# Performance work log

Measured on AMD Instinct MI355X. Metric: run time of the kernel, lower is better.

The kernel has to match this reference:

```python
import jax, jax.numpy as jnp
import numpy as np

ALPHA = 0.2  # leaky relu slope
NEG = -9e15

N, NFEAT, NHID, NHEADS = 4096, 1024, 64, 8
EMB = NHID * NHEADS  # 512


def setup_inputs() -> dict:
    key = jax.random.key(0)
    ks = jax.random.split(key, 16)
    x = jax.random.normal(ks[0], (N, NFEAT), dtype=jnp.float32)
    adj = (jax.random.uniform(ks[1], (N, N)) < 0.01).astype(jnp.float32)
    adj = jnp.maximum(adj, jnp.eye(N, dtype=jnp.float32))
    s = 0.05
    W = jax.random.normal(ks[2], (NHEADS, NFEAT, NHID), dtype=jnp.float32) * s
    a1 = jax.random.normal(ks[3], (NHEADS, NHID), dtype=jnp.float32) * s
    a2 = jax.random.normal(ks[4], (NHEADS, NHID), dtype=jnp.float32) * s
    # decoder: 512 -> 256 -> 256 -> 512 -> 1024 (PyTorch Linear convention: y = x @ W.T + b)
    W1 = jax.random.normal(ks[5], (EMB // 2, EMB), dtype=jnp.float32) * s
    b1 = jnp.zeros((EMB // 2,), dtype=jnp.float32)
    W2 = jax.random.normal(ks[6], (NFEAT // 4, EMB // 2), dtype=jnp.float32) * s
    b2 = jnp.zeros((NFEAT // 4,), dtype=jnp.float32)
    W3 = jax.random.normal(ks[7], (NFEAT // 2, NFEAT // 4), dtype=jnp.float32) * s
    b3 = jnp.zeros((NFEAT // 2,), dtype=jnp.float32)
    W4 = jax.random.normal(ks[8], (NFEAT, NFEAT // 2), dtype=jnp.float32) * s
    b4 = jnp.zeros((NFEAT,), dtype=jnp.float32)
    return {"x": x, "adj": adj, "W": W, "a1": a1, "a2": a2,
            "W1": W1, "b1": b1, "W2": W2, "b2": b2,
            "W3": W3, "b3": b3, "W4": W4, "b4": b4}


def reference(x, adj, W, a1, a2, W1, b1, W2, b2, W3, b3, W4, b4):
    # --- encoder: multi-head GAT (dropout=0) ---
    Wh = jnp.einsum('nf,hfd->hnd', x, W)              # [H, N, nhid]
    e_src = jnp.einsum('hnd,hd->hn', Wh, a1)          # [H, N]
    e_dst = jnp.einsum('hnd,hd->hn', Wh, a2)          # [H, N]
    e = jax.nn.leaky_relu(e_src[:, :, None] + e_dst[:, None, :], ALPHA)  # [H, N, N]
    e = jnp.where(adj[None] > 0, e, NEG)
    att = jax.nn.softmax(e, axis=-1)
    h = jnp.einsum('hnm,hmd->hnd', att, Wh)           # [H, N, nhid]
    h = jax.nn.elu(h)                                 # concat=True -> elu per layer
    enc = jnp.transpose(h, (1, 0, 2)).reshape(x.shape[0], -1)  # [N, H*nhid]
    # --- decoder: 4-layer MLP ---
    out = jax.nn.relu(enc @ W1.T + b1)
    out = jax.nn.relu(out @ W2.T + b2)
    out = jax.nn.relu(out @ W3.T + b3)
    out = out @ W4.T + b4
    return out
```

## Files before the change

### kernel.cpp

```cpp
#include <hip/hip_runtime.h>
#include <hip/hip_bf16.h>
#include <math.h>

#define NNODES 4096
#define NFEAT_ 1024
#define NHID_  64
#define NHEADS_ 8
#define EMB_   512
#define MAXD   256
constexpr float ALPHA_ = 0.2f;

typedef __attribute__((ext_vector_type(8))) short bf16x8;
typedef __attribute__((ext_vector_type(4))) float f32x4;
typedef unsigned int u32;
typedef unsigned short u16;

__device__ inline u16 f2b(float f) {
    __hip_bfloat16 b = __float2bfloat16(f);
    return *(u16*)&b;
}
__device__ inline float b2f(u16 u) {
    return __uint_as_float(((u32)u) << 16);
}

__device__ inline void cp16(const void* g, void* l) {
    __builtin_amdgcn_global_load_lds(
        (const __attribute__((address_space(1))) u32*)g,
        (__attribute__((address_space(3))) u32*)l, 16, 0, 0);
}

template<int BM, int BN, int OUTM, int ACT>
__global__ __launch_bounds__(256) void gemm_bt(
    const u16* __restrict__ A, const u16* __restrict__ B,
    const float* __restrict__ bias, void* __restrict__ Cv,
    int M, int N, int K)
{
    constexpr int BK  = 32;
    constexpr int WM  = BM / 2;
    constexpr int MI  = WM / 16;
    constexpr int WN  = BN / 2;
    constexpr int NJ  = WN / 16;
    constexpr int ACH = BM / 16;
    constexpr int BCH = BN / 16;

    __shared__ __align__(16) u16 As[2][BM * BK];
    __shared__ __align__(16) u16 Bs[2][BN * BK];

    const int tid  = threadIdx.x;
    const int wid  = tid >> 6, lane = tid & 63;
    const int wr   = wid >> 1, wc = wid & 1;
    const int m0   = blockIdx.y * BM, n0 = blockIdx.x * BN;
    const int frow = lane & 15, fk = (lane >> 4) * 8;
    const int lr   = lane >> 2, lc = (lane & 3) * 8;

    auto stage = [&](int buf, int k0) {
        const u16* gA = A + (long)m0 * K + k0;
        {
            int c = wid;
            cp16(gA + (long)(c * 16 + lr) * K + lc, &As[buf][c * 512]);
            if (ACH == 8) {
                c = wid + 4;
                cp16(gA + (long)(c * 16 + lr) * K + lc, &As[buf][c * 512]);
            }
        }
        const u16* gB = B + (long)n0 * K + k0;
        if (BCH >= 4) {
            int c = wid;
            cp16(gB + (long)(c * 16 + lr) * K + lc, &Bs[buf][c * 512]);
            if (BCH == 8) {
                c = wid + 4;
                cp16(gB + (long)(c * 16 + lr) * K + lc, &Bs[buf][c * 512]);
            }
        } else if (wid < BCH) {
            cp16(gB + (long)(wid * 16 + lr) * K + lc, &Bs[buf][wid * 512]);
        }
    };

    f32x4 acc[MI][NJ] = {};

    stage(0, 0);
    __syncthreads();
    int cur = 0;
    for (int k0 = 0; k0 < K; k0 += BK) {
        if (k0 + BK < K) stage(cur ^ 1, k0 + BK);

        bf16x8 af[MI], bfr[NJ];
        #pragma unroll
        for (int i = 0; i < MI; ++i)
            af[i] = *(const bf16x8*)&As[cur][(wr * WM + i * 16 + frow) * BK + fk];
        #pragma unroll
        for (int j = 0; j < NJ; ++j)
            bfr[j] = *(const bf16x8*)&Bs[cur][(wc * WN + j * 16 + frow) * BK + fk];
        #pragma unroll
        for (int i = 0; i < MI; ++i)
            #pragma unroll
            for (int j = 0; j < NJ; ++j)
                acc[i][j] = __builtin_amdgcn_mfma_f32_16x16x32_bf16(
                    af[i], bfr[j], acc[i][j], 0, 0, 0);

        __syncthreads();
        cur ^= 1;
    }

    const int crow0 = m0 + wr * WM + (lane >> 4) * 4;
    const int ccol0 = n0 + wc * WN + (lane & 15);
    #pragma unroll
    for (int i = 0; i < MI; ++i)
        #pragma unroll
        for (int j = 0; j < NJ; ++j)
            #pragma unroll
            for (int r = 0; r < 4; ++r) {
                const int row = crow0 + i * 16 + r;
                const int col = ccol0 + j * 16;
                float v = acc[i][j][r];
                if (bias) v += bias[col];
                if (ACT == 1) v = v > 0.f ? v : 0.f;
                if (OUTM == 1) ((u16*)Cv)[(long)row * N + col] = f2b(v);
                else           ((float*)Cv)[(long)row * N + col] = v;
            }
}

__global__ __launch_bounds__(256) void head_gemm_nbr(
    const u16* __restrict__ A, const u16* __restrict__ B,
    u16* __restrict__ Whb,
    const float* __restrict__ a1, const float* __restrict__ a2,
    float* __restrict__ es, float* __restrict__ edT,
    const float* __restrict__ adj, int* __restrict__ cnt,
    int* __restrict__ nbr)
{
    constexpr int BM = 64, BN = 64, BK = 32;
    constexpr int WM = 32, MI = 2, WN = 32, NJ = 2;
    constexpr int M = NNODES, N = EMB_, K = NFEAT_;

    __shared__ __align__(16) u16 As[2][BM * BK];
    __shared__ __align__(16) u16 Bs[2][BN * BK];
    __shared__ float s1Lds[2][BM];
    __shared__ float s2Lds[2][BM];
    __shared__ int lcnt;

    const int bid = blockIdx.x;
    const int tid = threadIdx.x;

    if (bid >= 512) {
        const int n = bid - 512;
        if (tid == 0) lcnt = 0;
        __syncthreads();
        const float4* arow = (const float4*)(adj + (long)n * NNODES);
        for (int m4 = tid; m4 < NNODES / 4; m4 += 256) {
            const float4 v = arow[m4];
            if (v.x != 0.f) { const int p = atomicAdd(&lcnt, 1); if (p < MAXD) nbr[n * MAXD + p] = m4 * 4; }
            if (v.y != 0.f) { const int p = atomicAdd(&lcnt, 1); if (p < MAXD) nbr[n * MAXD + p] = m4 * 4 + 1; }
            if (v.z != 0.f) { const int p = atomicAdd(&lcnt, 1); if (p < MAXD) nbr[n * MAXD + p] = m4 * 4 + 2; }
            if (v.w != 0.f) { const int p = atomicAdd(&lcnt, 1); if (p < MAXD) nbr[n * MAXD + p] = m4 * 4 + 3; }
        }
        __syncthreads();
        if (tid == 0) cnt[n] = lcnt < MAXD ? lcnt : MAXD;
        return;
    }

    const int wid  = tid >> 6, lane = tid & 63;
    const int wr   = wid >> 1, wc = wid & 1;
    const int m0   = (bid >> 3) * BM, n0 = (bid & 7) * BN;
    const int frow = lane & 15, fk = (lane >> 4) * 8;
    const int lr   = lane >> 2, lc = (lane & 3) * 8;

    auto stage = [&](int buf, int k0) {
        const u16* gA = A + (long)m0 * K + k0;
        cp16(gA + (long)(wid * 16 + lr) * K + lc, &As[buf][wid * 512]);
        const u16* gB = B + (long)n0 * K + k0;
        cp16(gB + (long)(wid * 16 + lr) * K + lc, &Bs[buf][wid * 512]);
    };

    f32x4 acc[MI][NJ] = {};

    stage(0, 0);
    __syncthreads();
    int cur = 0;
    for (int k0 = 0; k0 < K; k0 += BK) {
        if (k0 + BK < K) stage(cur ^ 1, k0 + BK);

        bf16x8 af[MI], bfr[NJ];
        #pragma unroll
        for (int i = 0; i < MI; ++i)
            af[i] = *(const bf16x8*)&As[cur][(wr * WM + i * 16 + frow) * BK + fk];
        #pragma unroll
        for (int j = 0; j < NJ; ++j)
            bfr[j] = *(const bf16x8*)&Bs[cur][(wc * WN + j * 16 + frow) * BK + fk];
        #pragma unroll
        for (int i = 0; i < MI; ++i)
            #pragma unroll
            for (int j = 0; j < NJ; ++j)
                acc[i][j] = __builtin_amdgcn_mfma_f32_16x16x32_bf16(
                    af[i], bfr[j], acc[i][j], 0, 0, 0);

        __syncthreads();
        cur ^= 1;
    }

    const int crow0 = m0 + wr * WM + (lane >> 4) * 4;
    const int ccol0 = n0 + wc * WN + (lane & 15);
    #pragma unroll
    for (int i = 0; i < MI; ++i)
        #pragma unroll
        for (int j = 0; j < NJ; ++j)
            #pragma unroll
            for (int r = 0; r < 4; ++r)
                Whb[(long)(crow0 + i * 16 + r) * N + ccol0 + j * 16] =
                    f2b(acc[i][j][r]);

    const int h = n0 >> 6;
    const float a1v0 = a1[h * 64 + wc * WN + frow];
    const float a1v1 = a1[h * 64 + wc * WN + 16 + frow];
    const float a2v0 = a2[h * 64 + wc * WN + frow];
    const float a2v1 = a2[h * 64 + wc * WN + 16 + frow];
    #pragma unroll
    for (int i = 0; i < MI; ++i)
        #pragma unroll
        for (int r = 0; r < 4; ++r) {
            float s1 = acc[i][0][r] * a1v0 + acc[i][1][r] * a1v1;
            float s2 = acc[i][0][r] * a2v0 + acc[i][1][r] * a2v1;
            #pragma unroll
            for (int off = 8; off; off >>= 1) {
                s1 += __shfl_xor(s1, off);
                s2 += __shfl_xor(s2, off);
            }
            if (frow == 0) {
                const int row = wr * WM + i * 16 + (lane >> 4) * 4 + r;
                s1Lds[wc][row] = s1;
                s2Lds[wc][row] = s2;
            }
        }
    __syncthreads();
    if (tid < BM) {
        es[h * NNODES + m0 + tid] = s1Lds[0][tid] + s1Lds[1][tid];
        edT[(m0 + tid) * NHEADS_ + h] = s2Lds[0][tid] + s2Lds[1][tid];
    }
}

#define CASTB 512
__global__ __launch_bounds__(256) void prep(
    const float* __restrict__ x,   const float* __restrict__ W,
    const float* __restrict__ W1,  const float* __restrict__ W2,
    const float* __restrict__ W3,  const float* __restrict__ W4,
    u16* __restrict__ xb,  u16* __restrict__ WcT,
    u16* __restrict__ W1b, u16* __restrict__ W2b,
    u16* __restrict__ W3b, u16* __restrict__ W4b)
{
    const int b = blockIdx.x, tid = threadIdx.x;

    if (b < CASTB) {
        const int np = CASTB * 256;
        const int t = b * 256 + tid;
        for (int i = t; i < (NNODES * NFEAT_) / 4; i += np) {
            const float4 v = ((const float4*)x)[i];
            ushort4 o; o.x = f2b(v.x); o.y = f2b(v.y); o.z = f2b(v.z); o.w = f2b(v.w);
            ((ushort4*)xb)[i] = o;
        }
        for (int i = t; i < (256 * 512) / 4; i += np) {
            const float4 v = ((const float4*)W1)[i];
            ushort4 o; o.x = f2b(v.x); o.y = f2b(v.y); o.z = f2b(v.z); o.w = f2b(v.w);
            ((ushort4*)W1b)[i] = o;
        }
        for (int i = t; i < (256 * 256) / 4; i += np) {
            const float4 v = ((const float4*)W2)[i];
            ushort4 o; o.x = f2b(v.x); o.y = f2b(v.y); o.z = f2b(v.z); o.w = f2b(v.w);
            ((ushort4*)W2b)[i] = o;
        }
        for (int i = t; i < (512 * 256) / 4; i += np) {
            const float4 v = ((const float4*)W3)[i];
            ushort4 o; o.x = f2b(v.x); o.y = f2b(v.y); o.z = f2b(v.z); o.w = f2b(v.w);
            ((ushort4*)W3b)[i] = o;
        }
        for (int i = t; i < (1024 * 512) / 4; i += np) {
            const float4 v = ((const float4*)W4)[i];
            ushort4 o; o.x = f2b(v.x); o.y = f2b(v.y); o.z = f2b(v.z); o.w = f2b(v.w);
            ((ushort4*)W4b)[i] = o;
        }
    } else {
        __shared__ float tile[64][65];
        const int tb = b - CASTB;
        const int h = tb >> 4, k0 = (tb & 15) * 64;
        #pragma unroll
        for (int p = 0; p < 4; ++p) {
            const int kr = p * 16 + (tid >> 4), d = (tid & 15) * 4;
            const float4 v = *(const float4*)&W[((long)h * NFEAT_ + k0 + kr) * NHID_ + d];
            tile[kr][d] = v.x; tile[kr][d + 1] = v.y;
            tile[kr][d + 2] = v.z; tile[kr][d + 3] = v.w;
        }
        __syncthreads();
        #pragma unroll
        for (int p = 0; p < 4; ++p) {
            const int d = p * 16 + (tid >> 4), k = (tid & 15) * 4;
            ushort4 o;
            o.x = f2b(tile[k][d]);     o.y = f2b(tile[k + 1][d]);
            o.z = f2b(tile[k + 2][d]); o.w = f2b(tile[k + 3][d]);
            *(ushort4*)&WcT[((long)h * 64 + d) * NFEAT_ + k0 + k] = o;
        }
    }
}

__global__ __launch_bounds__(512) void attn_agg(
    const u16* __restrict__ Whb, const float* __restrict__ esrc,
    const float* __restrict__ edT, const int* __restrict__ cnt,
    const int* __restrict__ nbr, u16* __restrict__ enc)
{
    __shared__ __align__(16) int   mLds[MAXD];
    __shared__ __align__(16) float pLds[NHEADS_][MAXD];
    const int h = threadIdx.x >> 6, lane = threadIdx.x & 63;
    const int n = blockIdx.x;

    const int deg  = min(cnt[n], MAXD);
    const int degp = (deg + 15) & ~15;

    if (h == 0) {
        const int* lst = nbr + n * MAXD;
        for (int j = lane; j < deg; j += 64) mLds[j] = lst[j];
        for (int j = deg + lane; j < degp; j += 64) mLds[j] = 0;
    }
    __syncthreads();

    const float es = esrc[h * NNODES + n];

    float mymax = -3.4e38f;
    for (int j = lane; j < deg; j += 64) {
        float ev = es + edT[mLds[j] * NHEADS_ + h];
        ev = ev > 0.f ? ev : ALPHA_ * ev;
        pLds[h][j] = ev;
        mymax = fmaxf(mymax, ev);
    }
    for (int j = deg + lane; j < degp; j += 64) pLds[h][j] = 0.f;
    #pragma unroll
    for (int off = 32; off; off >>= 1) mymax = fmaxf(mymax, __shfl_xor(mymax, off));

    float mysum = 0.f;
    for (int j = lane; j < deg; j += 64) {
        const float p = __expf(pLds[h][j] - mymax);
        pLds[h][j] = p;
        mysum += p;
    }
    #pragma unroll
    for (int off = 32; off; off >>= 1) mysum += __shfl_xor(mysum, off);

    __syncthreads();

    float acc = 0.f;
    const u16* base = Whb + h * NHID_ + lane;
    for (int j0 = 0; j0 < degp; j0 += 16) {
        const int4   ma = *(const int4*)&mLds[j0];
        const int4   mb = *(const int4*)&mLds[j0 + 4];
        const int4   mc = *(const int4*)&mLds[j0 + 8];
        const int4   md = *(const int4*)&mLds[j0 + 12];
        const float4 pa = *(const float4*)&pLds[h][j0];
        const float4 pb = *(const float4*)&pLds[h][j0 + 4];
        const float4 pc = *(const float4*)&pLds[h][j0 + 8];
        const float4 pd = *(const float4*)&pLds[h][j0 + 12];
        const float v0  = b2f(base[(long)ma.x << 9]);
        const float v1  = b2f(base[(long)ma.y << 9]);
        const float v2  = b2f(base[(long)ma.z << 9]);
        const float v3  = b2f(base[(long)ma.w << 9]);
        const float v4  = b2f(base[(long)mb.x << 9]);
        const float v5  = b2f(base[(long)mb.y << 9]);
        const float v6  = b2f(base[(long)mb.z << 9]);
        const float v7  = b2f(base[(long)mb.w << 9]);
        const float v8  = b2f(base[(long)mc.x << 9]);
        const float v9  = b2f(base[(long)mc.y << 9]);
        const float v10 = b2f(base[(long)mc.z << 9]);
        const float v11 = b2f(base[(long)mc.w << 9]);
        const float v12 = b2f(base[(long)md.x << 9]);
        const float v13 = b2f(base[(long)md.y << 9]);
        const float v14 = b2f(base[(long)md.z << 9]);
        const float v15 = b2f(base[(long)md.w << 9]);
        acc = fmaf(pa.x, v0,  acc); acc = fmaf(pa.y, v1,  acc);
        acc = fmaf(pa.z, v2,  acc); acc = fmaf(pa.w, v3,  acc);
        acc = fmaf(pb.x, v4,  acc); acc = fmaf(pb.y, v5,  acc);
        acc = fmaf(pb.z, v6,  acc); acc = fmaf(pb.w, v7,  acc);
        acc = fmaf(pc.x, v8,  acc); acc = fmaf(pc.y, v9,  acc);
        acc = fmaf(pc.z, v10, acc); acc = fmaf(pc.w, v11, acc);
        acc = fmaf(pd.x, v12, acc); acc = fmaf(pd.y, v13, acc);
        acc = fmaf(pd.z, v14, acc); acc = fmaf(pd.w, v15, acc);
    }

    float hv = acc / mysum;
    hv = hv > 0.f ? hv : expm1f(hv);
    enc[(long)n * EMB_ + h * NHID_ + lane] = f2b(hv);
}

extern "C" void kernel_launch(void* const* d_in, const int* in_sizes, int n_in,
                              void* d_out, int out_size, void* d_ws, size_t ws_size,
                              hipStream_t stream)
{
    const float* x   = (const float*)d_in[0];
    const float* adj = (const float*)d_in[1];
    const float* W   = (const float*)d_in[2];
    const float* a1  = (const float*)d_in[3];
    const float* a2  = (const float*)d_in[4];
    const float* W1  = (const float*)d_in[5];
    const float* b1  = (const float*)d_in[6];
    const float* W2  = (const float*)d_in[7];
    const float* b2  = (const float*)d_in[8];
    const float* W3  = (const float*)d_in[9];
    const float* b3  = (const float*)d_in[10];
    const float* W4  = (const float*)d_in[11];
    const float* b4  = (const float*)d_in[12];
    float* out = (float*)d_out;

    float* es  = (float*)d_ws;
    float* edT = es + 32768;
    u16* Whb = (u16*)(edT + 32768);
    u16* enc = Whb + 2097152;
    u16* WcT = enc + 2097152;
    u16* W1b = WcT + 524288;
    u16* W2b = W1b + 131072;
    u16* W3b = W2b + 65536;
    u16* W4b = W3b + 131072;
    int* cnt = (int*)(W4b + 524288);
    int* nbr = cnt + 4096;
    u16* xb  = (u16*)(nbr + 1048576);
    u16* dd1 = xb;
    u16* dd2 = dd1 + 1048576;
    u16* dd3 = dd2 + 1048576;

    prep<<<dim3(CASTB + 128), 256, 0, stream>>>(
        x, W, W1, W2, W3, W4, xb, WcT, W1b, W2b, W3b, W4b);

    head_gemm_nbr<<<dim3(512 + NNODES), 256, 0, stream>>>(
        xb, WcT, Whb, a1, a2, es, edT, adj, cnt, nbr);

    attn_agg<<<dim3(NNODES), 512, 0, stream>>>(Whb, es, edT, cnt, nbr, enc);

    gemm_bt<64, 32, 1, 1><<<dim3(8, 64), 256, 0, stream>>>(
        enc, W1b, b1, dd1, NNODES, 256, 512);
    gemm_bt<64, 32, 1, 1><<<dim3(8, 64), 256, 0, stream>>>(
        dd1, W2b, b2, dd2, NNODES, 256, 256);
    gemm_bt<64, 64, 1, 1><<<dim3(8, 64), 256, 0, stream>>>(
        dd2, W3b, b3, dd3, NNODES, 512, 256);
    gemm_bt<64, 128, 0, 0><<<dim3(8, 64), 256, 0, stream>>>(
        dd3, W4b, b4, out, NNODES, 1024, 512);
}
```

Before: 222.1 us.

## Fuse four decoder GEMMs into one cooperative kernel with grid syncs

The four separate decoder MLP GEMM launches become one cooperative kernel of 512 blocks. Each block computes its tile for every layer in turn, with a grid-wide barrier between layers. This removes three kernel launch gaps and the tail idle time between layers. In exchange it adds grid.sync costs and needs the whole grid co-resident, and the shared LDS is sized for the largest tile, which may lower occupancy.

Result: slower. 419.1 us (+88.7%).

```diff
diff --git a/kernel.cpp b/kernel.cpp
--- a/kernel.cpp
+++ b/kernel.cpp
@@ -1,6 +1,9 @@
 #include <hip/hip_runtime.h>
+#include <hip/hip_cooperative_groups.h>
 #include <hip/hip_bf16.h>
 #include <math.h>
+
+namespace cg = cooperative_groups;
 
 #define NNODES 4096
 #define NFEAT_ 1024
@@ -30,10 +33,11 @@
 }
 
 template<int BM, int BN, int OUTM, int ACT>
-__global__ __launch_bounds__(256) void gemm_bt(
+__device__ __forceinline__ void gemm_tile(
+    u16* __restrict__ As, u16* __restrict__ Bs,
     const u16* __restrict__ A, const u16* __restrict__ B,
     const float* __restrict__ bias, void* __restrict__ Cv,
-    int M, int N, int K)
+    int N, int K, int bid)
 {
     constexpr int BK  = 32;
     constexpr int WM  = BM / 2;
@@ -42,14 +46,12 @@
     constexpr int NJ  = WN / 16;
     constexpr int ACH = BM / 16;
     constexpr int BCH = BN / 16;
-
-    __shared__ __align__(16) u16 As[2][BM * BK];
-    __shared__ __align__(16) u16 Bs[2][BN * BK];
+    constexpr int ASZ = BM * BK, BSZ = BN * BK;
 
     const int tid  = threadIdx.x;
     const int wid  = tid >> 6, lane = tid & 63;
     const int wr   = wid >> 1, wc = wid & 1;
-    const int m0   = blockIdx.y * BM, n0 = blockIdx.x * BN;
+    const int m0   = (bid >> 3) * BM, n0 = (bid & 7) * BN;
     const int frow = lane & 15, fk = (lane >> 4) * 8;
     const int lr   = lane >> 2, lc = (lane & 3) * 8;
 
@@ -57,22 +59,22 @@
         const u16* gA = A + (long)m0 * K + k0;
         {
             int c = wid;
-            cp16(gA + (long)(c * 16 + lr) * K + lc, &As[buf][c * 512]);
+            cp16(gA + (long)(c * 16 + lr) * K + lc, &As[buf * ASZ + c * 512]);
             if (ACH == 8) {
                 c = wid + 4;
-                cp16(gA + (long)(c * 16 + lr) * K + lc, &As[buf][c * 512]);
+                cp16(gA + (long)(c * 16 + lr) * K + lc, &As[buf * ASZ + c * 512]);
             }
         }
         const u16* gB = B + (long)n0 * K + k0;
         if (BCH >= 4) {
             int c = wid;
-            cp16(gB + (long)(c * 16 + lr) * K + lc, &Bs[buf][c * 512]);
+            cp16(gB + (long)(c * 16 + lr) * K + lc, &Bs[buf * BSZ + c * 512]);
             if (BCH == 8) {
                 c = wid + 4;
-                cp16(gB + (long)(c * 16 + lr) * K + lc, &Bs[buf][c * 512]);
+                cp16(gB + (long)(c * 16 + lr) * K + lc, &Bs[buf * BSZ + c * 512]);
             }
         } else if (wid < BCH) {
-            cp16(gB + (long)(wid * 16 + lr) * K + lc, &Bs[buf][wid * 512]);
+            cp16(gB + (long)(wid * 16 + lr) * K + lc, &Bs[buf * BSZ + wid * 512]);
         }
     };
 
@@ -87,10 +89,10 @@
         bf16x8 af[MI], bfr[NJ];
         #pragma unroll
         for (int i = 0; i < MI; ++i)
-            af[i] = *(const bf16x8*)&As[cur][(wr * WM + i * 16 + frow) * BK + fk];
+            af[i] = *(const bf16x8*)&As[cur * ASZ + (wr * WM + i * 16 + frow) * BK + fk];
         #pragma unroll
         for (int j = 0; j < NJ; ++j)
-            bfr[j] = *(const bf16x8*)&Bs[cur][(wc * WN + j * 16 + frow) * BK + fk];
+            bfr[j] = *(const bf16x8*)&Bs[cur * BSZ + (wc * WN + j * 16 + frow) * BK + fk];
         #pragma unroll
         for (int i = 0; i < MI; ++i)
             #pragma unroll
@@ -120,6 +122,27 @@
             }
 }
 
+__global__ __launch_bounds__(256) void decoder_fused(
+    const u16* __restrict__ enc,
+    const u16* __restrict__ W1b, const float* __restrict__ b1, u16* __restrict__ dd1,
+    const u16* __restrict__ W2b, const float* __restrict__ b2, u16* __restrict__ dd2,
+    const u16* __restrict__ W3b, const float* __restrict__ b3, u16* __restrict__ dd3,
+    const u16* __restrict__ W4b, const float* __restrict__ b4, float* __restrict__ out)
+{
+    __shared__ __align__(16) u16 As[2 * 64 * 32];
+    __shared__ __align__(16) u16 Bs[2 * 128 * 32];
+    cg::grid_group grid = cg::this_grid();
+    const int bid = blockIdx.x;
+
+    gemm_tile<64, 32, 1, 1>(As, Bs, enc, W1b, b1, dd1, 256, 512, bid);
+    grid.sync();
+    gemm_tile<64, 32, 1, 1>(As, Bs, dd1, W2b, b2, dd2, 256, 256, bid);
+    grid.sync();
+    gemm_tile<64, 64, 1, 1>(As, Bs, dd2, W3b, b3, dd3, 512, 256, bid);
+    grid.sync();
+    gemm_tile<64, 128, 0, 0>(As, Bs, dd3, W4b, b4, out, 1024, 512, bid);
+}
+
 __global__ __launch_bounds__(256) void head_gemm_nbr(
     const u16* __restrict__ A, const u16* __restrict__ B,
     u16* __restrict__ Whb,
@@ -130,7 +153,7 @@
 {
     constexpr int BM = 64, BN = 64, BK = 32;
     constexpr int WM = 32, MI = 2, WN = 32, NJ = 2;
-    constexpr int M = NNODES, N = EMB_, K = NFEAT_;
+    constexpr int N = EMB_, K = NFEAT_;
 
     __shared__ __align__(16) u16 As[2][BM * BK];
     __shared__ __align__(16) u16 Bs[2][BN * BK];
@@ -428,12 +451,16 @@
 
     attn_agg<<<dim3(NNODES), 512, 0, stream>>>(Whb, es, edT, cnt, nbr, enc);
 
-    gemm_bt<64, 32, 1, 1><<<dim3(8, 64), 256, 0, stream>>>(
-        enc, W1b, b1, dd1, NNODES, 256, 512);
-    gemm_bt<64, 32, 1, 1><<<dim3(8, 64), 256, 0, stream>>>(
-        dd1, W2b, b2, dd2, NNODES, 256, 256);
-    gemm_bt<64, 64, 1, 1><<<dim3(8, 64), 256, 0, stream>>>(
-        dd2, W3b, b3, dd3, NNODES, 512, 256);
-    gemm_bt<64, 128, 0, 0><<<dim3(8, 64), 256, 0, stream>>>(
-        dd3, W4b, b4, out, NNODES, 1024, 512);
-}
+    {
+        const u16* enc_c = enc;
+        void* kargs[] = {
+            (void*)&enc_c,
+            (void*)&W1b, (void*)&b1, (void*)&dd1,
+            (void*)&W2b, (void*)&b2, (void*)&dd2,
+            (void*)&W3b, (void*)&b3, (void*)&dd3,
+            (void*)&W4b, (void*)&b4, (void*)&out
+        };
+        hipLaunchCooperativeKernel((const void*)decoder_fused,
+                                   dim3(512), dim3(256), kargs, 0, stream);
+    }
+}
```
